# Optimization experiments

Measured on AMD Instinct MI355X. Metric: run time of the kernel, lower is better.

Reference implementation:

```python
import jax, jax.numpy as jnp
import numpy as np

N_NODES = 100_000
N_EDGES = 6_400_000
CH = 5


def setup_inputs() -> dict:
    key = jax.random.key(0)
    ks = jax.random.split(key, 16)
    inp = {
        "x": jax.random.normal(ks[0], (N_NODES, 2), dtype=jnp.float32),
        "edge_index": jax.random.randint(ks[1], (2, N_EDGES), 0, N_NODES, dtype=jnp.int64 if jax.config.jax_enable_x64 else jnp.int32).astype(jnp.int32),
        "edge_attr": jax.random.uniform(ks[2], (N_EDGES, 1), dtype=jnp.float32),
        "lin1_w": jax.random.normal(ks[3], (2, CH), dtype=jnp.float32) * 0.5,
        "lin1_b": jax.random.normal(ks[4], (CH,), dtype=jnp.float32) * 0.1,
        "conv1_wf": jax.random.normal(ks[5], (2 * CH + 1, CH), dtype=jnp.float32) * 0.3,
        "conv1_bf": jax.random.normal(ks[6], (CH,), dtype=jnp.float32) * 0.1,
        "conv1_ws": jax.random.normal(ks[7], (2 * CH + 1, CH), dtype=jnp.float32) * 0.3,
        "conv1_bs": jax.random.normal(ks[8], (CH,), dtype=jnp.float32) * 0.1,
        "conv2_wf": jax.random.normal(ks[9], (2 * CH + 1, CH), dtype=jnp.float32) * 0.3,
        "conv2_bf": jax.random.normal(ks[10], (CH,), dtype=jnp.float32) * 0.1,
        "conv2_ws": jax.random.normal(ks[11], (2 * CH + 1, CH), dtype=jnp.float32) * 0.3,
        "conv2_bs": jax.random.normal(ks[12], (CH,), dtype=jnp.float32) * 0.1,
        "lin2_w": jax.random.normal(ks[13], (CH, 2), dtype=jnp.float32) * 0.5,
        "lin2_b": jax.random.normal(ks[14], (2,), dtype=jnp.float32) * 0.1,
    }
    return inp


def cgconv(x, edge_index, edge_attr, wf, bf, ws, bs):
    # PyG CGConv: x_i' = x_i + sum_{j->i} sigmoid(z W_f + b_f) * softplus(z W_s + b_s)
    # z = [x_i, x_j, e_ij]; edge_index[0]=source j, edge_index[1]=target i
    src, dst = edge_index[0], edge_index[1]
    z = jnp.concatenate([x[dst], x[src], edge_attr], axis=-1)  # [E, 2C+dim]
    msg = jax.nn.sigmoid(z @ wf + bf) * jax.nn.softplus(z @ ws + bs)  # [E, C]
    agg = jax.ops.segment_sum(msg, dst, num_segments=x.shape[0])  # [N, C]
    return x + agg


def reference(x, edge_index, edge_attr,
              lin1_w, lin1_b,
              conv1_wf, conv1_bf, conv1_ws, conv1_bs,
              conv2_wf, conv2_bf, conv2_ws, conv2_bs,
              lin2_w, lin2_b):
    h = x @ lin1_w + lin1_b  # [N, C]
    h = cgconv(h, edge_index, edge_attr, conv1_wf, conv1_bf, conv1_ws, conv1_bs)
    h = cgconv(h, edge_index, edge_attr, conv2_wf, conv2_bf, conv2_ws, conv2_bs)
    return h @ lin2_w + lin2_b  # [N, 2]
```

## Files before the change

kernel.cpp:

```cpp
#include <hip/hip_runtime.h>
#include <hip/hip_fp16.h>

constexpr int NN = 100000;
constexpr int NE = 6400000;
constexpr int BSH = 7;
constexpr int BN = 1 << BSH;
constexpr int NBUCK = (NN + BN - 1) / BN;
constexpr int BCAP = 9216;
constexpr int STILE = 8192;
constexpr int NSB = (NE + STILE - 1) / STILE;
constexpr int NP = 1024;

#define LOG2E 1.44269504f
#define LN2   0.69314718f


__global__ __launch_bounds__(256) void k_lin2(const float* __restrict__ h,
                                              const float* __restrict__ w,
                                              const float* __restrict__ b,
                                              float* __restrict__ out) {
    int n = blockIdx.x * 256 + threadIdx.x;
    if (n >= NN) return;
    float o0 = b[0], o1 = b[1];
#pragma unroll
    for (int c = 0; c < 5; ++c) {
        float hv = h[(size_t)n * 5 + c];
        o0 += hv * w[2 * c];
        o1 += hv * w[2 * c + 1];
    }
    out[2 * n] = o0;
    out[2 * n + 1] = o1;
}

__device__ __forceinline__ void prep_core(const float hv[5],
                                          const float* __restrict__ wf,
                                          const float* __restrict__ bf,
                                          const float* __restrict__ ws,
                                          const float* __restrict__ bs,
                                          int n, float* __restrict__ TD,
                                          unsigned short* __restrict__ TSh) {
    float tg[5], ts[5], sg[5], ss[5];
#pragma unroll
    for (int c = 0; c < 5; ++c) {
        float a = bf[c], d = bs[c], u = 0.f, v = 0.f;
#pragma unroll
        for (int k = 0; k < 5; ++k) {
            a += hv[k] * wf[k * 5 + c];
            d += hv[k] * ws[k * 5 + c];
            u += hv[k] * wf[(5 + k) * 5 + c];
            v += hv[k] * ws[(5 + k) * 5 + c];
        }
        tg[c] = -a * LOG2E; ts[c] = -d * LOG2E;
        sg[c] = -u * LOG2E; ss[c] = -v * LOG2E;
    }
    float4* Dp = (float4*)(TD + (size_t)n * 12);
    Dp[0] = make_float4(tg[0], tg[1], tg[2], tg[3]);
    Dp[1] = make_float4(tg[4], ts[0], ts[1], ts[2]);
    Dp[2] = make_float4(ts[3], ts[4], 0.f, 0.f);

    unsigned p[5];
#pragma unroll
    for (int c = 0; c < 5; ++c) {
        unsigned lo = (unsigned)__half_as_ushort(__float2half_rn(sg[c]));
        unsigned hi = (unsigned)__half_as_ushort(__float2half_rn(ss[c]));
        p[c] = lo | (hi << 16);
    }
    uint4 w0 = make_uint4(p[0], p[1], p[2], p[3]);
    uint4 w1 = make_uint4(p[4], 0u, 0u, 0u);
    *(uint4*)(TSh + (size_t)n * 16) = w0;
    *(uint4*)(TSh + (size_t)n * 16 + 8) = w1;
}

__global__ __launch_bounds__(256) void k_prep1(const float* __restrict__ x,
                                               const float* __restrict__ l1w,
                                               const float* __restrict__ l1b,
                                               const float* __restrict__ wf,
                                               const float* __restrict__ bf,
                                               const float* __restrict__ ws,
                                               const float* __restrict__ bs,
                                               float* __restrict__ TD,
                                               unsigned short* __restrict__ TSh,
                                               float* __restrict__ h) {
    int n = blockIdx.x * 256 + threadIdx.x;
    if (n >= NN) return;
    float x0 = x[2 * n], x1 = x[2 * n + 1];
    float hv[5];
#pragma unroll
    for (int c = 0; c < 5; ++c) {
        hv[c] = l1b[c] + x0 * l1w[c] + x1 * l1w[5 + c];
        h[(size_t)n * 5 + c] = hv[c];
    }
    prep_core(hv, wf, bf, ws, bs, n, TD, TSh);
}

__global__ __launch_bounds__(256) void k_prep(const float* __restrict__ h,
                                              const float* __restrict__ wf,
                                              const float* __restrict__ bf,
                                              const float* __restrict__ ws,
                                              const float* __restrict__ bs,
                                              float* __restrict__ TD,
                                              unsigned short* __restrict__ TSh) {
    int n = blockIdx.x * 256 + threadIdx.x;
    if (n >= NN) return;
    float hv[5];
#pragma unroll
    for (int k = 0; k < 5; ++k) hv[k] = h[(size_t)n * 5 + k];
    prep_core(hv, wf, bf, ws, bs, n, TD, TSh);
}

__global__ __launch_bounds__(256) void k_initcurs(int* __restrict__ gcurs) {
    int i = blockIdx.x * 256 + threadIdx.x;
    if (i < NBUCK) gcurs[i] = i * BCAP;
}

__global__ __launch_bounds__(512) void k_scatter4(const int* __restrict__ ei,
                                                  const float* __restrict__ ea,
                                                  int* __restrict__ gcurs,
                                                  unsigned int* __restrict__ rec) {
    __shared__ unsigned int lrec[STILE];
    __shared__ unsigned int spk[STILE];
    __shared__ int C[NBUCK];
    __shared__ int loc[NBUCK];
    __shared__ int gbase[NBUCK];
    __shared__ int A[NP];
    const int tid = threadIdx.x, blk = blockIdx.x;
    const int base = blk * STILE;
    const int m = min(STILE, NE - base);

    for (int i = tid; i < NBUCK; i += 512) C[i] = 0;
    __syncthreads();

    const int m4 = m >> 2;
    const int4* s4 = (const int4*)(ei + base);
    const int4* d4 = (const int4*)(ei + NE + base);
    const float4* a4 = (const float4*)(ea + base);
    for (int q = tid; q < m4; q += 512) {
        int4 s = s4[q];
        int4 d = d4[q];
        float4 a = a4[q];
        int k = q * 4;
        lrec[k + 0] = (unsigned)s.x | ((unsigned)(d.x & (BN - 1)) << 17) |
                      (__float2uint_rn(a.x * 255.f) << 24);
        lrec[k + 1] = (unsigned)s.y | ((unsigned)(d.y & (BN - 1)) << 17) |
                      (__float2uint_rn(a.y * 255.f) << 24);
        lrec[k + 2] = (unsigned)s.z | ((unsigned)(d.z & (BN - 1)) << 17) |
                      (__float2uint_rn(a.z * 255.f) << 24);
        lrec[k + 3] = (unsigned)s.w | ((unsigned)(d.w & (BN - 1)) << 17) |
                      (__float2uint_rn(a.w * 255.f) << 24);
        atomicAdd(&C[(unsigned)d.x >> BSH], 1);
        atomicAdd(&C[(unsigned)d.y >> BSH], 1);
        atomicAdd(&C[(unsigned)d.z >> BSH], 1);
        atomicAdd(&C[(unsigned)d.w >> BSH], 1);
    }
    __syncthreads();

    for (int b = tid; b < NBUCK; b += 512)
        gbase[b] = C[b] ? atomicAdd(&gcurs[b], C[b]) : 0;
    for (int i = tid; i < NP; i += 512) A[i] = (i < NBUCK) ? C[i] : 0;
    __syncthreads();

    for (int d = 1; d < NP; d <<= 1) {
        int i = (tid + 1) * (d << 1) - 1;
        if (i < NP) A[i] += A[i - d];
        __syncthreads();
    }
    if (tid == 0) A[NP - 1] = 0;
    __syncthreads();
    for (int d = NP >> 1; d >= 1; d >>= 1) {
        int i = (tid + 1) * (d << 1) - 1;
        if (i < NP) { int t = A[i - d]; A[i - d] = A[i]; A[i] += t; }
        __syncthreads();
    }
    for (int b = tid; b < NBUCK; b += 512) loc[b] = A[b];
    __syncthreads();

    for (int k = tid; k < m; k += 512) {
        int bkt = (unsigned)ei[NE + base + k] >> BSH;
        int p = atomicAdd(&loc[bkt], 1);
        spk[p] = (unsigned)k | ((unsigned)bkt << 16);
    }
    __syncthreads();

    for (int p = tid; p < m; p += 512) {
        unsigned pk = spk[p];
        int k = pk & 0xFFFF;
        int bkt = pk >> 16;
        rec[gbase[bkt] + (p - A[bkt])] = lrec[k];
    }
}

__global__ __launch_bounds__(512) void k_sortbkt(const int* __restrict__ gcurs,
                                                 unsigned int* __restrict__ rec,
                                                 int2* __restrict__ nrange) {
    __shared__ unsigned int lrec[BCAP];
    __shared__ int cnt[BN];
    __shared__ int curs[BN];
    const int b = blockIdx.x, tid = threadIdx.x;
    const int e0 = b * BCAP;
    const int m = gcurs[b] - e0;
    const int node0 = b << BSH;
    const int nloc = min(BN, NN - node0);

    for (int i = tid; i < m; i += 512) lrec[i] = rec[e0 + i];
    if (tid < BN) cnt[tid] = 0;
    __syncthreads();
    for (int i = tid; i < m; i += 512)
        atomicAdd(&cnt[(lrec[i] >> 17) & (BN - 1)], 1);
    __syncthreads();
    int v = (tid < BN) ? cnt[tid] : 0;
    for (int off = 1; off < BN; off <<= 1) {
        int t = 0;
        if (tid < BN && tid >= off) t = cnt[tid - off];
        __syncthreads();
        if (tid < BN) cnt[tid] += t;
        __syncthreads();
    }
    if (tid < BN) {
        int excl = cnt[tid] - v;
        curs[tid] = excl;
        if (tid < nloc)
            nrange[node0 + tid] = make_int2(e0 + excl, e0 + excl + v);
    }
    __syncthreads();
    for (int i = tid; i < m; i += 512) {
        unsigned int r = lrec[i];
        int dl = (r >> 17) & (BN - 1);
        int pos = atomicAdd(&curs[dl], 1);
        rec[e0 + pos] = r;
    }
}

__global__ __launch_bounds__(256) void k_conv_csr(
        const unsigned int* __restrict__ rec, const int2* __restrict__ nrange,
        const float* __restrict__ TD, const unsigned short* __restrict__ TSh,
        const float* __restrict__ wf, const float* __restrict__ ws,
        float* __restrict__ h ) {
    const int tid = threadIdx.x;
    const int lane = tid & 15;
    const int g = tid >> 4;
    const int nbase = blockIdx.x * 64;

    __half2 we2[5];
#pragma unroll
    for (int c = 0; c < 5; ++c)
        we2[c] = __floats2half2_rn(-wf[50 + c] * LOG2E, -ws[50 + c] * LOG2E);
    const __half2 one2 = __float2half2_rn(1.f);
    const __half hz = __float2half(0.f);

#pragma unroll
    for (int ni = 0; ni < 4; ++ni) {
        const int n = nbase + ni * 16 + g;
        if (n >= NN) continue;

        const float4* Dp = (const float4*)(TD + (size_t)n * 12);
        float4 d0 = Dp[0], d1 = Dp[1], d2 = Dp[2];
        __half2 dd2[5];
        dd2[0] = __floats2half2_rn(d0.x, d1.y);
        dd2[1] = __floats2half2_rn(d0.y, d1.z);
        dd2[2] = __floats2half2_rn(d0.z, d1.w);
        dd2[3] = __floats2half2_rn(d0.w, d2.x);
        dd2[4] = __floats2half2_rn(d1.x, d2.y);

        float acc[5] = {0.f, 0.f, 0.f, 0.f, 0.f};
        const int2 rg = nrange[n];
        const int eEnd = rg.y;
        for (int e = rg.x + lane; e < eEnd; e += 64) {
            unsigned r[4];
            bool vld[4];
            float4 q0[4];
            unsigned q1[4];
            __half2 a2[4];
#pragma unroll
            for (int j = 0; j < 4; ++j) {
                int ej = e + j * 16;
                vld[j] = ej < eEnd;
                r[j] = rec[vld[j] ? ej : e];
            }
#pragma unroll
            for (int j = 0; j < 4; ++j) {
                const unsigned src = r[j] & 0x1FFFFu;
                const unsigned short* row = TSh + (size_t)src * 16;
                q0[j] = *(const float4*)row;
                q1[j] = *(const unsigned*)(row + 8);
                a2[j] = __float2half2_rn((float)(r[j] >> 24) * (1.f / 255.f));
            }
#pragma unroll
            for (int j = 0; j < 4; ++j) {
                if (!vld[j]) continue;
                union { float4 f; __half2 h2[4]; } u; u.f = q0[j];
                __half2 s2[5] = {u.h2[0], u.h2[1], u.h2[2], u.h2[3],
                                 *(__half2*)&q1[j]};
#pragma unroll
                for (int c = 0; c < 5; ++c) {
                    __half2 z2 = __hadd2(__hfma2(a2[j], we2[c], dd2[c]), s2[c]);
                    __half zx = __low2half(z2);
                    __half zy = __high2half(z2);
                    __half nab = __hmin(zy, __hneg(zy));
                    __half2 e2 = h2exp2(__halves2half2(zx, nab));
                    __half2 o2 = __hadd2(e2, one2);
                    float sig = __half2float(hrcp(__low2half(o2)));
                    float lg  = __half2float(hlog2(__high2half(o2)));
                    float mx  = __half2float(__hmin(zy, hz));
                    acc[c] = fmaf(sig, lg - mx, acc[c]);
                }
            }
        }
#pragma unroll
        for (int off = 8; off >= 1; off >>= 1)
#pragma unroll
            for (int c = 0; c < 5; ++c)
                acc[c] += __shfl_xor(acc[c], off, 16);
        if (lane == 0) {
#pragma unroll
            for (int c = 0; c < 5; ++c)
                h[(size_t)n * 5 + c] += LN2 * acc[c];
        }
    }
}

__global__ __launch_bounds__(256) void k_prep_fb(const float* __restrict__ h,
                                                 const float* __restrict__ wf,
                                                 const float* __restrict__ bf,
                                                 const float* __restrict__ ws,
                                                 const float* __restrict__ bs,
                                                 float* __restrict__ T,
                                                 float* __restrict__ S,
                                                 float* __restrict__ hout) {
    int n = blockIdx.x * 256 + threadIdx.x;
    if (n >= NN) return;
    float hv[5];
#pragma unroll
    for (int k = 0; k < 5; ++k) hv[k] = h[5 * n + k];
    float tf[5], ts[5], sf[5], ss[5];
#pragma unroll
    for (int c = 0; c < 5; ++c) {
        float a = bf[c], d = bs[c], u = 0.f, v = 0.f;
#pragma unroll
        for (int k = 0; k < 5; ++k) {
            a += hv[k] * wf[k * 5 + c];
            d += hv[k] * ws[k * 5 + c];
            u += hv[k] * wf[(5 + k) * 5 + c];
            v += hv[k] * ws[(5 + k) * 5 + c];
        }
        tf[c] = a; ts[c] = d; sf[c] = u; ss[c] = v;
    }
    float4* Tp = (float4*)(T + (size_t)n * 16);
    Tp[0] = make_float4(tf[0], tf[1], tf[2], tf[3]);
    Tp[1] = make_float4(tf[4], ts[0], ts[1], ts[2]);
    Tp[2] = make_float4(ts[3], ts[4], 0.f, 0.f);
    float4* Sp = (float4*)(S + (size_t)n * 16);
    Sp[0] = make_float4(sf[0], sf[1], sf[2], sf[3]);
    Sp[1] = make_float4(sf[4], ss[0], ss[1], ss[2]);
    Sp[2] = make_float4(ss[3], ss[4], 0.f, 0.f);
#pragma unroll
    for (int c = 0; c < 5; ++c) hout[5 * n + c] = hv[c];
}

__global__ __launch_bounds__(256) void k_conv_atomic(const int* __restrict__ ei,
                                                     const float* __restrict__ ea,
                                                     const float* __restrict__ T,
                                                     const float* __restrict__ S,
                                                     const float* __restrict__ wf,
                                                     const float* __restrict__ ws,
                                                     float* __restrict__ hout) {
    int e = blockIdx.x * 256 + threadIdx.x;
    if (e >= NE) return;
    int src = ei[e];
    int dst = ei[NE + e];
    float a = ea[e];
    const float4* Tp = (const float4*)(T + (size_t)dst * 16);
    const float4* Sp = (const float4*)(S + (size_t)src * 16);
    float4 t0 = Tp[0], t1 = Tp[1], t2 = Tp[2];
    float4 s0 = Sp[0], s1 = Sp[1], s2 = Sp[2];
    float za[5] = {t0.x + s0.x, t0.y + s0.y, t0.z + s0.z, t0.w + s0.w, t1.x + s1.x};
    float zs[5] = {t1.y + s1.y, t1.z + s1.z, t1.w + s1.w, t2.x + s2.x, t2.y + s2.y};
    float* outp = hout + (size_t)dst * 5;
#pragma unroll
    for (int c = 0; c < 5; ++c) {
        float f = za[c] + a * wf[50 + c];
        float s = zs[c] + a * ws[50 + c];
        float sig = 1.f / (1.f + __expf(-f));
        float sp = __logf(1.f + __expf(-fabsf(s))) + fmaxf(s, 0.f);
        unsafeAtomicAdd(outp + c, sig * sp);
    }
}

__global__ __launch_bounds__(256) void k_lin1_fb(const float* __restrict__ x,
                                                 const float* __restrict__ w,
                                                 const float* __restrict__ b,
                                                 float* __restrict__ h) {
    int n = blockIdx.x * 256 + threadIdx.x;
    if (n >= NN) return;
    float x0 = x[2 * n], x1 = x[2 * n + 1];
#pragma unroll
    for (int c = 0; c < 5; ++c)
        h[5 * n + c] = b[c] + x0 * w[c] + x1 * w[5 + c];
}

extern "C" void kernel_launch(void* const* d_in, const int* in_sizes, int n_in,
                              void* d_out, int out_size, void* d_ws, size_t ws_size,
                              hipStream_t stream) {
    const float* x    = (const float*)d_in[0];
    const int*   ei   = (const int*)d_in[1];
    const float* ea   = (const float*)d_in[2];
    const float* l1w  = (const float*)d_in[3];
    const float* l1b  = (const float*)d_in[4];
    const float* c1wf = (const float*)d_in[5];
    const float* c1bf = (const float*)d_in[6];
    const float* c1ws = (const float*)d_in[7];
    const float* c1bs = (const float*)d_in[8];
    const float* c2wf = (const float*)d_in[9];
    const float* c2bf = (const float*)d_in[10];
    const float* c2ws = (const float*)d_in[11];
    const float* c2bs = (const float*)d_in[12];
    const float* l2w  = (const float*)d_in[13];
    const float* l2b  = (const float*)d_in[14];
    float* out = (float*)d_out;
    char* ws = (char*)d_ws;

    size_t o_rec    = 0;
    size_t o_nrange = o_rec + (size_t)NBUCK * BCAP * 4;
    size_t o_gcurs  = o_nrange + (size_t)NN * 8;
    size_t o_TD     = (o_gcurs + (size_t)NBUCK * 4 + 15) & ~(size_t)15;
    size_t o_TS     = o_TD + (size_t)NN * 12 * 4;
    size_t o_h      = o_TS + (size_t)NN * 16 * 2;
    size_t need     = o_h + (size_t)NN * 5 * 4;

    int nb_n = (NN + 255) / 256;

    if (ws_size >= need) {
        unsigned int* rec    = (unsigned int*)(ws + o_rec);
        int2* nrange         = (int2*)(ws + o_nrange);
        int* gcurs           = (int*)(ws + o_gcurs);
        float* TD            = (float*)(ws + o_TD);
        unsigned short* TSh  = (unsigned short*)(ws + o_TS);
        float* h             = (float*)(ws + o_h);

        k_initcurs<<<(NBUCK + 255) / 256, 256, 0, stream>>>(gcurs);
        k_scatter4<<<NSB,   512, 0, stream>>>(ei, ea, gcurs, rec);
        k_sortbkt <<<NBUCK, 512, 0, stream>>>(gcurs, rec, nrange);

        k_prep1<<<nb_n, 256, 0, stream>>>(x, l1w, l1b,
                                          c1wf, c1bf, c1ws, c1bs, TD, TSh, h);
        k_conv_csr<<<(NN + 63) / 64, 256, 0, stream>>>(rec, nrange, TD, TSh,
                                                       c1wf, c1ws, h);
        k_prep<<<nb_n, 256, 0, stream>>>(h, c2wf, c2bf, c2ws, c2bs, TD, TSh);
        k_conv_csr<<<(NN + 63) / 64, 256, 0, stream>>>(rec, nrange, TD, TSh,
                                                       c2wf, c2ws, h);
        k_lin2<<<nb_n, 256, 0, stream>>>(h, l2w, l2b, out);
    } else {
        float* h0 = (float*)(ws);
        float* h1 = (float*)(ws + 2000000);
        float* h2 = h0;
        float* T  = (float*)(ws + 4000000);
        float* S  = (float*)(ws + 10400000);
        int nb_e = (NE + 255) / 256;

        k_lin1_fb<<<nb_n, 256, 0, stream>>>(x, l1w, l1b, h0);
        k_prep_fb<<<nb_n, 256, 0, stream>>>(h0, c1wf, c1bf, c1ws, c1bs, T, S, h1);
        k_conv_atomic<<<nb_e, 256, 0, stream>>>(ei, ea, T, S, c1wf, c1ws, h1);
        k_prep_fb<<<nb_n, 256, 0, stream>>>(h1, c2wf, c2bf, c2ws, c2bs, T, S, h2);
        k_conv_atomic<<<nb_e, 256, 0, stream>>>(ei, ea, T, S, c2wf, c2ws, h2);
        k_lin2<<<nb_n, 256, 0, stream>>>(h2, l2w, l2b, out);
    }
}
```

Measured before the change: 213.6 us.

## Fuse layer-2 prep into conv1 and lin2 into conv2, double-buffer tables

Conv1 now also computes the second layer's per-node tables (TD2/TS2) right after aggregation, which removes the separate prep kernel. Conv2 applies the final linear layer directly, which removes k_lin2. Separate table buffers are needed because conv1 still reads TD1/TS1 while writing the layer-2 tables. The conv blocks now handle 16 nodes each instead of looping over 64, which changes the grid shape and load balance. The in-block node-range check is gone, which is only safe because NN is divisible by 16.

```diff
diff --git a/kernel.cpp b/kernel.cpp
--- a/kernel.cpp
+++ b/kernel.cpp
@@ -14,23 +14,6 @@
 #define LOG2E 1.44269504f
 #define LN2   0.69314718f
 
-
-__global__ __launch_bounds__(256) void k_lin2(const float* __restrict__ h,
-                                              const float* __restrict__ w,
-                                              const float* __restrict__ b,
-                                              float* __restrict__ out) {
-    int n = blockIdx.x * 256 + threadIdx.x;
-    if (n >= NN) return;
-    float o0 = b[0], o1 = b[1];
-#pragma unroll
-    for (int c = 0; c < 5; ++c) {
-        float hv = h[(size_t)n * 5 + c];
-        o0 += hv * w[2 * c];
-        o1 += hv * w[2 * c + 1];
-    }
-    out[2 * n] = o0;
-    out[2 * n + 1] = o1;
-}
 
 __device__ __forceinline__ void prep_core(const float hv[5],
                                           const float* __restrict__ wf,
@@ -90,21 +73,6 @@
         hv[c] = l1b[c] + x0 * l1w[c] + x1 * l1w[5 + c];
         h[(size_t)n * 5 + c] = hv[c];
     }
-    prep_core(hv, wf, bf, ws, bs, n, TD, TSh);
-}
-
-__global__ __launch_bounds__(256) void k_prep(const float* __restrict__ h,
-                                              const float* __restrict__ wf,
-                                              const float* __restrict__ bf,
-                                              const float* __restrict__ ws,
-                                              const float* __restrict__ bs,
-                                              float* __restrict__ TD,
-                                              unsigned short* __restrict__ TSh) {
-    int n = blockIdx.x * 256 + threadIdx.x;
-    if (n >= NN) return;
-    float hv[5];
-#pragma unroll
-    for (int k = 0; k < 5; ++k) hv[k] = h[(size_t)n * 5 + k];
     prep_core(hv, wf, bf, ws, bs, n, TD, TSh);
 }
 
@@ -230,91 +198,149 @@
     }
 }
 
-__global__ __launch_bounds__(256) void k_conv_csr(
+__device__ __forceinline__ void conv_core(
+        const unsigned int* __restrict__ rec, const int2 rg,
+        const float4* __restrict__ Dp, const unsigned short* __restrict__ TSh,
+        const __half2 we2[5], float acc[5]) {
+    const int lane = threadIdx.x & 15;
+    float4 d0 = Dp[0], d1 = Dp[1], d2 = Dp[2];
+    __half2 dd2[5];
+    dd2[0] = __floats2half2_rn(d0.x, d1.y);
+    dd2[1] = __floats2half2_rn(d0.y, d1.z);
+    dd2[2] = __floats2half2_rn(d0.z, d1.w);
+    dd2[3] = __floats2half2_rn(d0.w, d2.x);
+    dd2[4] = __floats2half2_rn(d1.x, d2.y);
+    const __half2 one2 = __float2half2_rn(1.f);
+    const __half hz = __float2half(0.f);
+
+#pragma unroll
+    for (int c = 0; c < 5; ++c) acc[c] = 0.f;
+    const int eEnd = rg.y;
+    for (int e = rg.x + lane; e < eEnd; e += 64) {
+        unsigned r[4];
+        bool vld[4];
+        float4 q0[4];
+        unsigned q1[4];
+        __half2 a2[4];
+#pragma unroll
+        for (int j = 0; j < 4; ++j) {
+            int ej = e + j * 16;
+            vld[j] = ej < eEnd;
+            r[j] = rec[vld[j] ? ej : e];
+        }
+#pragma unroll
+        for (int j = 0; j < 4; ++j) {
+            const unsigned src = r[j] & 0x1FFFFu;
+            const unsigned short* row = TSh + (size_t)src * 16;
+            q0[j] = *(const float4*)row;
+            q1[j] = *(const unsigned*)(row + 8);
+            a2[j] = __float2half2_rn((float)(r[j] >> 24) * (1.f / 255.f));
+        }
+#pragma unroll
+        for (int j = 0; j < 4; ++j) {
+            if (!vld[j]) continue;
+            union { float4 f; __half2 h2[4]; } u; u.f = q0[j];
+            __half2 s2[5] = {u.h2[0], u.h2[1], u.h2[2], u.h2[3],
+                             *(__half2*)&q1[j]};
+#pragma unroll
+            for (int c = 0; c < 5; ++c) {
+                __half2 z2 = __hadd2(__hfma2(a2[j], we2[c], dd2[c]), s2[c]);
+                __half zx = __low2half(z2);
+                __half zy = __high2half(z2);
+                __half nab = __hmin(zy, __hneg(zy));
+                __half2 e2 = h2exp2(__halves2half2(zx, nab));
+                __half2 o2 = __hadd2(e2, one2);
+                float sig = __half2float(hrcp(__low2half(o2)));
+                float lg  = __half2float(hlog2(__high2half(o2)));
+                float mx  = __half2float(__hmin(zy, hz));
+                acc[c] = fmaf(sig, lg - mx, acc[c]);
+            }
+        }
+    }
+#pragma unroll
+    for (int off = 8; off >= 1; off >>= 1)
+#pragma unroll
+        for (int c = 0; c < 5; ++c)
+            acc[c] += __shfl_xor(acc[c], off, 16);
+}
+
+__global__ __launch_bounds__(256) void k_conv_prep(
         const unsigned int* __restrict__ rec, const int2* __restrict__ nrange,
         const float* __restrict__ TD, const unsigned short* __restrict__ TSh,
         const float* __restrict__ wf, const float* __restrict__ ws,
-        float* __restrict__ h ) {
+        const float* __restrict__ wf2, const float* __restrict__ bf2,
+        const float* __restrict__ ws2, const float* __restrict__ bs2,
+        float* __restrict__ h,
+        float* __restrict__ TD2, unsigned short* __restrict__ TSh2) {
     const int tid = threadIdx.x;
     const int lane = tid & 15;
-    const int g = tid >> 4;
-    const int nbase = blockIdx.x * 64;
+    const int n = blockIdx.x * 16 + (tid >> 4);
 
     __half2 we2[5];
 #pragma unroll
     for (int c = 0; c < 5; ++c)
         we2[c] = __floats2half2_rn(-wf[50 + c] * LOG2E, -ws[50 + c] * LOG2E);
-    const __half2 one2 = __float2half2_rn(1.f);
-    const __half hz = __float2half(0.f);
-
-#pragma unroll
-    for (int ni = 0; ni < 4; ++ni) {
-        const int n = nbase + ni * 16 + g;
-        if (n >= NN) continue;
-
-        const float4* Dp = (const float4*)(TD + (size_t)n * 12);
-        float4 d0 = Dp[0], d1 = Dp[1], d2 = Dp[2];
-        __half2 dd2[5];
-        dd2[0] = __floats2half2_rn(d0.x, d1.y);
-        dd2[1] = __floats2half2_rn(d0.y, d1.z);
-        dd2[2] = __floats2half2_rn(d0.z, d1.w);
-        dd2[3] = __floats2half2_rn(d0.w, d2.x);
-        dd2[4] = __floats2half2_rn(d1.x, d2.y);
-
-        float acc[5] = {0.f, 0.f, 0.f, 0.f, 0.f};
-        const int2 rg = nrange[n];
-        const int eEnd = rg.y;
-        for (int e = rg.x + lane; e < eEnd; e += 64) {
-            unsigned r[4];
-            bool vld[4];
-            float4 q0[4];
-            unsigned q1[4];
-            __half2 a2[4];
-#pragma unroll
-            for (int j = 0; j < 4; ++j) {
-                int ej = e + j * 16;
-                vld[j] = ej < eEnd;
-                r[j] = rec[vld[j] ? ej : e];
-            }
-#pragma unroll
-            for (int j = 0; j < 4; ++j) {
-                const unsigned src = r[j] & 0x1FFFFu;
-                const unsigned short* row = TSh + (size_t)src * 16;
-                q0[j] = *(const float4*)row;
-                q1[j] = *(const unsigned*)(row + 8);
-                a2[j] = __float2half2_rn((float)(r[j] >> 24) * (1.f / 255.f));
-            }
-#pragma unroll
-            for (int j = 0; j < 4; ++j) {
-                if (!vld[j]) continue;
-                union { float4 f; __half2 h2[4]; } u; u.f = q0[j];
-                __half2 s2[5] = {u.h2[0], u.h2[1], u.h2[2], u.h2[3],
-                                 *(__half2*)&q1[j]};
-#pragma unroll
-                for (int c = 0; c < 5; ++c) {
-                    __half2 z2 = __hadd2(__hfma2(a2[j], we2[c], dd2[c]), s2[c]);
-                    __half zx = __low2half(z2);
-                    __half zy = __high2half(z2);
-                    __half nab = __hmin(zy, __hneg(zy));
-                    __half2 e2 = h2exp2(__halves2half2(zx, nab));
-                    __half2 o2 = __hadd2(e2, one2);
-                    float sig = __half2float(hrcp(__low2half(o2)));
-                    float lg  = __half2float(hlog2(__high2half(o2)));
-                    float mx  = __half2float(__hmin(zy, hz));
-                    acc[c] = fmaf(sig, lg - mx, acc[c]);
-                }
-            }
-        }
-#pragma unroll
-        for (int off = 8; off >= 1; off >>= 1)
-#pragma unroll
-            for (int c = 0; c < 5; ++c)
-                acc[c] += __shfl_xor(acc[c], off, 16);
-        if (lane == 0) {
-#pragma unroll
-            for (int c = 0; c < 5; ++c)
-                h[(size_t)n * 5 + c] += LN2 * acc[c];
-        }
+
+    float acc[5];
+    conv_core(rec, nrange[n], (const float4*)(TD + (size_t)n * 12), TSh,
+              we2, acc);
+
+    float hv[5];
+#pragma unroll
+    for (int c = 0; c < 5; ++c)
+        hv[c] = h[(size_t)n * 5 + c] + LN2 * acc[c];
+    if (lane == 0) {
+#pragma unroll
+        for (int c = 0; c < 5; ++c) h[(size_t)n * 5 + c] = hv[c];
+    }
+    if (lane < 5) {
+        const int c = lane;
+        float a = bf2[c], d = bs2[c], u = 0.f, v = 0.f;
+#pragma unroll
+        for (int k = 0; k < 5; ++k) {
+            a += hv[k] * wf2[k * 5 + c];
+            d += hv[k] * ws2[k * 5 + c];
+            u += hv[k] * wf2[(5 + k) * 5 + c];
+            v += hv[k] * ws2[(5 + k) * 5 + c];
+        }
+        TD2[(size_t)n * 12 + c]     = -a * LOG2E;
+        TD2[(size_t)n * 12 + 5 + c] = -d * LOG2E;
+        unsigned lo = (unsigned)__half_as_ushort(__float2half_rn(-u * LOG2E));
+        unsigned hi = (unsigned)__half_as_ushort(__float2half_rn(-v * LOG2E));
+        ((unsigned*)(TSh2 + (size_t)n * 16))[c] = lo | (hi << 16);
+    }
+}
+
+__global__ __launch_bounds__(256) void k_conv_out(
+        const unsigned int* __restrict__ rec, const int2* __restrict__ nrange,
+        const float* __restrict__ TD, const unsigned short* __restrict__ TSh,
+        const float* __restrict__ wf, const float* __restrict__ ws,
+        const float* __restrict__ h,
+        const float* __restrict__ l2w, const float* __restrict__ l2b,
+        float* __restrict__ out) {
+    const int tid = threadIdx.x;
+    const int lane = tid & 15;
+    const int n = blockIdx.x * 16 + (tid >> 4);
+
+    __half2 we2[5];
+#pragma unroll
+    for (int c = 0; c < 5; ++c)
+        we2[c] = __floats2half2_rn(-wf[50 + c] * LOG2E, -ws[50 + c] * LOG2E);
+
+    float acc[5];
+    conv_core(rec, nrange[n], (const float4*)(TD + (size_t)n * 12), TSh,
+              we2, acc);
+
+    if (lane == 0) {
+        float o0 = l2b[0], o1 = l2b[1];
+#pragma unroll
+        for (int c = 0; c < 5; ++c) {
+            float hv = h[(size_t)n * 5 + c] + LN2 * acc[c];
+            o0 += hv * l2w[2 * c];
+            o1 += hv * l2w[2 * c + 1];
+        }
+        out[2 * n] = o0;
+        out[2 * n + 1] = o1;
     }
 }
 
@@ -395,6 +421,23 @@
 #pragma unroll
     for (int c = 0; c < 5; ++c)
         h[5 * n + c] = b[c] + x0 * w[c] + x1 * w[5 + c];
+}
+
+__global__ __launch_bounds__(256) void k_lin2_fb(const float* __restrict__ h,
+                                                 const float* __restrict__ w,
+                                                 const float* __restrict__ b,
+                                                 float* __restrict__ out) {
+    int n = blockIdx.x * 256 + threadIdx.x;
+    if (n >= NN) return;
+    float o0 = b[0], o1 = b[1];
+#pragma unroll
+    for (int c = 0; c < 5; ++c) {
+        float hv = h[(size_t)n * 5 + c];
+        o0 += hv * w[2 * c];
+        o1 += hv * w[2 * c + 1];
+    }
+    out[2 * n] = o0;
+    out[2 * n + 1] = o1;
 }
 
 extern "C" void kernel_launch(void* const* d_in, const int* in_sizes, int n_in,
@@ -421,9 +464,11 @@
     size_t o_rec    = 0;
     size_t o_nrange = o_rec + (size_t)NBUCK * BCAP * 4;
     size_t o_gcurs  = o_nrange + (size_t)NN * 8;
-    size_t o_TD     = (o_gcurs + (size_t)NBUCK * 4 + 15) & ~(size_t)15;
-    size_t o_TS     = o_TD + (size_t)NN * 12 * 4;
-    size_t o_h      = o_TS + (size_t)NN * 16 * 2;
+    size_t o_TD1    = (o_gcurs + (size_t)NBUCK * 4 + 15) & ~(size_t)15;
+    size_t o_TS1    = o_TD1 + (size_t)NN * 12 * 4;
+    size_t o_TD2    = o_TS1 + (size_t)NN * 16 * 2;
+    size_t o_TS2    = o_TD2 + (size_t)NN * 12 * 4;
+    size_t o_h      = o_TS2 + (size_t)NN * 16 * 2;
     size_t need     = o_h + (size_t)NN * 5 * 4;
 
     int nb_n = (NN + 255) / 256;
@@ -432,8 +477,10 @@
         unsigned int* rec    = (unsigned int*)(ws + o_rec);
         int2* nrange         = (int2*)(ws + o_nrange);
         int* gcurs           = (int*)(ws + o_gcurs);
-        float* TD            = (float*)(ws + o_TD);
-        unsigned short* TSh  = (unsigned short*)(ws + o_TS);
+        float* TD1           = (float*)(ws + o_TD1);
+        unsigned short* TS1  = (unsigned short*)(ws + o_TS1);
+        float* TD2           = (float*)(ws + o_TD2);
+        unsigned short* TS2  = (unsigned short*)(ws + o_TS2);
         float* h             = (float*)(ws + o_h);
 
         k_initcurs<<<(NBUCK + 255) / 256, 256, 0, stream>>>(gcurs);
@@ -441,13 +488,13 @@
         k_sortbkt <<<NBUCK, 512, 0, stream>>>(gcurs, rec, nrange);
 
         k_prep1<<<nb_n, 256, 0, stream>>>(x, l1w, l1b,
-                                          c1wf, c1bf, c1ws, c1bs, TD, TSh, h);
-        k_conv_csr<<<(NN + 63) / 64, 256, 0, stream>>>(rec, nrange, TD, TSh,
-                                                       c1wf, c1ws, h);
-        k_prep<<<nb_n, 256, 0, stream>>>(h, c2wf, c2bf, c2ws, c2bs, TD, TSh);
-        k_conv_csr<<<(NN + 63) / 64, 256, 0, stream>>>(rec, nrange, TD, TSh,
-                                                       c2wf, c2ws, h);
-        k_lin2<<<nb_n, 256, 0, stream>>>(h, l2w, l2b, out);
+                                          c1wf, c1bf, c1ws, c1bs, TD1, TS1, h);
+        k_conv_prep<<<NN / 16, 256, 0, stream>>>(rec, nrange, TD1, TS1,
+                                                 c1wf, c1ws,
+                                                 c2wf, c2bf, c2ws, c2bs,
+                                                 h, TD2, TS2);
+        k_conv_out<<<NN / 16, 256, 0, stream>>>(rec, nrange, TD2, TS2,
+                                                c2wf, c2ws, h, l2w, l2b, out);
     } else {
         float* h0 = (float*)(ws);
         float* h1 = (float*)(ws + 2000000);
@@ -461,6 +508,6 @@
         k_conv_atomic<<<nb_e, 256, 0, stream>>>(ei, ea, T, S, c1wf, c1ws, h1);
         k_prep_fb<<<nb_n, 256, 0, stream>>>(h1, c2wf, c2bf, c2ws, c2bs, T, S, h2);
         k_conv_atomic<<<nb_e, 256, 0, stream>>>(ei, ea, T, S, c2wf, c2ws, h2);
-        k_lin2<<<nb_n, 256, 0, stream>>>(h2, l2w, l2b, out);
-    }
-}
+        k_lin2_fb<<<nb_n, 256, 0, stream>>>(h2, l2w, l2b, out);
+    }
+}
```

Result: faster. 190.6 us (-10.8%).
